# Kernel tuning notes

Hardware: AMD Instinct MI355X
Metric: run time of the kernel (lower is better)

The kernel has to match this reference:

```python
import jax, jax.numpy as jnp
import numpy as np

B, N_C, N_T, D, DF = 16, 2048, 1024, 2, 2
K, E_OBS = 16, 4
H, DH = 4, 16
F = H * DH  # 64-dim node features (embed_all output)


def setup_inputs() -> dict:
    key = jax.random.key(0)
    ks = jax.random.split(key, 16)
    r = lambda i, shape: jax.random.normal(ks[i], shape, jnp.float32) * 0.05
    d_in = E_OBS + D + DF  # obs(4) + s(2) + f(2) = 8
    return dict(
        s_ctx=jax.random.normal(ks[0], (B, N_C, D), jnp.float32),
        f_ctx=jax.random.normal(ks[1], (B, N_C, DF), jnp.float32),
        s_test=jax.random.normal(ks[2], (B, N_T, D), jnp.float32),
        emb_obs=r(3, (2, E_OBS)),
        W1=r(4, (d_in, 256)), b1=jnp.zeros((256,), jnp.float32),
        W2=r(5, (256, 128)), b2=jnp.zeros((128,), jnp.float32),
        W3=r(6, (128, F)), b3=jnp.zeros((F,), jnp.float32),
        ln_g=jnp.ones((F,), jnp.float32), ln_b=jnp.zeros((F,), jnp.float32),
        Wg=r(7, (F, F)),
        a_src=r(8, (H, DH)), a_dst=r(9, (H, DH)),
        We=r(10, (D, H)), be=jnp.zeros((H,), jnp.float32),
        H1=r(11, (F, 256)), c1=jnp.zeros((256,), jnp.float32),
        H2=r(12, (256, 64)), c2=jnp.zeros((64,), jnp.float32),
        H3=r(13, (64, 2)), c3=jnp.zeros((2,), jnp.float32),
    )


def _knn(q, ctx, k):
    # q [B,Nq,D], ctx [B,Nc,D] -> neighbor indices [B,Nq,K] and displacement edge feats [B,Nq,K,D]
    d2 = (jnp.sum(q * q, -1)[:, :, None] + jnp.sum(ctx * ctx, -1)[:, None, :]
          - 2.0 * jnp.einsum('bqd,bcd->bqc', q, ctx))
    _, idx = jax.lax.top_k(-d2, k)
    nb = jax.vmap(lambda c, i: c[i])(ctx, idx)  # gather neighbor coords per batch
    return idx, q[:, :, None, :] - nb


def _mlp3(x, W1, b1, W2, b2, W3, b3):
    x = jax.nn.gelu(x @ W1 + b1)
    x = jax.nn.gelu(x @ W2 + b2)
    return x @ W3 + b3


def _ln(x, g, b):
    mu = jnp.mean(x, -1, keepdims=True)
    v = jnp.var(x, -1, keepdims=True)
    return (x - mu) * jax.lax.rsqrt(v + 1e-6) * g + b


def reference(s_ctx, f_ctx, s_test, emb_obs, W1, b1, W2, b2, W3, b3, ln_g, ln_b,
              Wg, a_src, a_dst, We, be, H1, c1, H2, c2, H3, c3):
    # --- build kNN graph (ctx->ctx and ctx->test edges, K per receiver) ---
    s_cc, d_cc = _knn(s_ctx, s_ctx, K)
    s_ct, d_ct = _knn(s_test, s_ctx, K)
    edges = jnp.concatenate([d_cc.reshape(-1, D), d_ct.reshape(-1, D)], axis=0)  # [E, D]
    off = (jnp.arange(B) * N_C)[:, None, None]
    senders = jnp.concatenate([(s_cc + off).reshape(-1), (s_ct + off).reshape(-1)])  # [E]
    # receivers == repeat(arange(N), K): edges are grouped K-per-node in node order.

    # --- node embedding: [obs_embed | s | f] -> MLP -> LayerNorm ---
    ctx_in = jnp.concatenate([jnp.broadcast_to(emb_obs[1], (B, N_C, E_OBS)), s_ctx, f_ctx], -1)
    test_in = jnp.concatenate([jnp.broadcast_to(emb_obs[0], (B, N_T, E_OBS)), s_test,
                               jnp.zeros((B, N_T, DF), s_test.dtype)], -1)
    n_ctx = _ln(_mlp3(ctx_in, W1, b1, W2, b2, W3, b3), ln_g, ln_b)
    n_test = _ln(_mlp3(test_in, W1, b1, W2, b2, W3, b3), ln_g, ln_b)
    nodes = jnp.concatenate([n_ctx.reshape(B * N_C, F), n_test.reshape(B * N_T, F)], 0)
    N = B * (N_C + N_T)

    # --- edge-biased GAT message passing (K incoming edges per node) ---
    xp = (nodes @ Wg).reshape(N, H, DH)
    msg = xp[senders].reshape(N, K, H, DH)  # gather sender features
    sc = (jnp.einsum('nkhd,hd->nkh', msg, a_src)
          + jnp.einsum('nhd,hd->nh', xp, a_dst)[:, None, :])
    sc = jax.nn.leaky_relu(sc, 0.2) + (edges @ We + be).reshape(N, K, H)  # edge bias
    alpha = jax.nn.softmax(sc, axis=1)  # softmax over the K neighbors
    out = jnp.einsum('nkh,nkhd->nhd', alpha, msg).reshape(N, F)
    nodes = nodes + out  # residual

    # --- head on test nodes + diagonal MVN output ---
    n_t = nodes[-B * N_T:].reshape(B, N_T, F)
    o = jax.nn.gelu(n_t @ H1 + c1)
    o = jax.nn.gelu(o @ H2 + c2)
    o = o @ H3 + c3  # [B, N_t, 2]
    mean = o[..., 0:1]
    scale = jax.nn.softplus(o[..., 1:2])
    return jnp.concatenate([mean, scale], -1)
```

## Files before the change

### kernel.cpp

```cpp
#include <hip/hip_runtime.h>
#include <math.h>

#define NB 16
#define NCTX 2048
#define NTEST 1024
#define NCTX_TOT (NB*NCTX)
#define NTEST_TOT (NB*NTEST)
#define NTOT (NCTX_TOT + NTEST_TOT)

typedef _Float16 half8 __attribute__((ext_vector_type(8)));
typedef _Float16 half4 __attribute__((ext_vector_type(4)));
typedef float f32x4 __attribute__((ext_vector_type(4)));

__device__ __forceinline__ float gelu_f(float x) {
  float x3 = x * x * x;
  float y = 0.7978845608028654f * fmaf(0.044715f, x3, x);
  float e = __expf(2.0f * y);
  float th = 1.0f - 2.0f * __builtin_amdgcn_rcpf(e + 1.0f);
  return 0.5f * x * (1.0f + th);
}

__device__ __forceinline__ void fma4(float4& a, float s, float4 w) {
  a.x = fmaf(s, w.x, a.x);
  a.y = fmaf(s, w.y, a.y);
  a.z = fmaf(s, w.z, a.z);
  a.w = fmaf(s, w.w, a.w);
}

__device__ __forceinline__ float4 ldg4(const float* p) {
  return *reinterpret_cast<const float4*>(p);
}

__device__ __forceinline__ unsigned fkey(float f) {
  unsigned u = __float_as_uint(f);
  return (u & 0x80000000u) ? ~u : (u ^ 0x80000000u);
}
__device__ __forceinline__ float unfkey(unsigned k) {
  return (k & 0x80000000u) ? __uint_as_float(k ^ 0x80000000u)
                           : __uint_as_float(~k);
}

__global__ __launch_bounds__(256) void prep_kernel(
    const float* __restrict__ W1, const float* __restrict__ b1,
    const float* __restrict__ emb,
    const float* __restrict__ W2, const float* __restrict__ W3,
    const float* __restrict__ Wg,
    const float* __restrict__ H1, const float* __restrict__ H2,
    _Float16* __restrict__ W2P, _Float16* __restrict__ W3P,
    _Float16* __restrict__ WgP,
    _Float16* __restrict__ H1P, _Float16* __restrict__ H2P,
    float* __restrict__ ctype)
{
  int t = blockIdx.x * 256 + threadIdx.x;
  {
    int j = t >> 9, ks = (t >> 6) & 7, l = t & 63;
    int col = 16*j + (l & 15);
    int k0  = ks*32 + (l >> 4)*8;
    half8 o;
    #pragma unroll
    for (int e = 0; e < 8; ++e) o[e] = (_Float16)W2[(k0 + e)*128 + col];
    *reinterpret_cast<half8*>(&W2P[(size_t)t*8]) = o;
  }
  if (t < 1024) {
    int j = t >> 8, ks = (t >> 6) & 3, l = t & 63;
    int col = 16*j + (l & 15);
    int k0  = ks*32 + (l >> 4)*8;
    half8 o;
    #pragma unroll
    for (int e = 0; e < 8; ++e) o[e] = (_Float16)W3[(k0 + e)*64 + col];
    *reinterpret_cast<half8*>(&W3P[(size_t)t*8]) = o;
  }
  if (t < 512) {
    int j = t >> 7, ks = (t >> 6) & 1, l = t & 63;
    int col = 16*j + (l & 15);
    int k0  = ks*32 + (l >> 4)*8;
    half8 o;
    #pragma unroll
    for (int e = 0; e < 8; ++e) o[e] = (_Float16)Wg[(k0 + e)*64 + col];
    *reinterpret_cast<half8*>(&WgP[(size_t)t*8]) = o;
  }
  if (t < 2048) {
    int j = t >> 7, ks = (t >> 6) & 1, l = t & 63;
    int col = 16*j + (l & 15);
    int k0  = ks*32 + (l >> 4)*8;
    half8 o;
    #pragma unroll
    for (int e = 0; e < 8; ++e) o[e] = (_Float16)H1[(k0 + e)*256 + col];
    *reinterpret_cast<half8*>(&H1P[(size_t)t*8]) = o;
  }
  if (t < 2048) {
    int j = t >> 9, ks = (t >> 6) & 7, l = t & 63;
    int col = 16*j + (l & 15);
    int k0  = ks*32 + (l >> 4)*8;
    half8 o;
    #pragma unroll
    for (int e = 0; e < 8; ++e) o[e] = (_Float16)H2[(k0 + e)*64 + col];
    *reinterpret_cast<half8*>(&H2P[(size_t)t*8]) = o;
  }
  if (t < 512) {
    int ty = t >> 8, c = t & 255;
    float acc = b1[c];
    #pragma unroll
    for (int k = 0; k < 4; ++k) acc = fmaf(emb[ty*4 + k], W1[k*256 + c], acc);
    ctype[t] = acc;
  }
}

__global__ __launch_bounds__(256, 6) void knn_kernel(
    const float* __restrict__ s_ctx, const float* __restrict__ s_test,
    int* __restrict__ senders)
{
  __shared__ __align__(16) unsigned long long sk[4][128];
  const int t    = threadIdx.x;
  const int lane = t & 63;
  const int w    = t >> 6;
  const int blk  = blockIdx.x;
  const int bb   = blk >> 8;
  const int q    = (blk & 255) * 4 + w;
  const int trow = bb * NTEST + q;

  const float* cb = s_ctx + (size_t)bb * NCTX * 2;
  const float qx = s_test[(size_t)trow*2];
  const float qy = s_test[(size_t)trow*2 + 1];
  const float qq = __fadd_rn(__fmul_rn(qx,qx), __fmul_rn(qy,qy));

  float d[32];
  float mn = 3.4e38f;
  #pragma unroll
  for (int it = 0; it < 32; ++it) {
    float2 p = *reinterpret_cast<const float2*>(&cb[2*(it*64 + lane)]);
    float ss  = __fadd_rn(__fmul_rn(p.x,p.x), __fmul_rn(p.y,p.y));
    float dot = __fadd_rn(__fmul_rn(qx, p.x), __fmul_rn(qy, p.y));
    float d2  = __fsub_rn(__fadd_rn(qq, ss), __fmul_rn(2.0f, dot));
    d[it] = d2;
    mn = fminf(mn, d2);
  }

  unsigned key = fkey(mn);
  unsigned acc = 0u;
  #pragma unroll
  for (int bit = 31; bit >= 0; --bit) {
    unsigned candv = acc | (1u << bit);
    unsigned long long bal = __ballot(key < candv);
    if (__popcll(bal) < 16) acc = candv;
  }
  const float Tf = unfkey(acc);

  int base = 0;
  #pragma unroll
  for (int it = 0; it < 32; ++it) {
    bool pr = (d[it] <= Tf);
    unsigned long long m = __ballot(pr);
    if (pr) {
      int pos = base + __popcll(m & ((1ULL << lane) - 1ULL));
      if (pos < 128)
        sk[w][pos] = ((unsigned long long)fkey(d[it]) << 32)
                   | (unsigned)(it*64 + lane);
    }
    base += __popcll(m);
  }
  const int S = base;

  if (S <= 32) {
    if (lane >= S && lane < 32) sk[w][lane] = ~0ULL;
    unsigned long long pm = sk[w][lane & 31];
    int r0 = 0;
    #pragma unroll
    for (int j = 0; j < 32; ++j)
      r0 += (int)(sk[w][j] < pm);
    if (lane < S && r0 < 16)
      senders[(size_t)trow*16 + r0] = bb*NCTX + (int)(pm & 0xFFFFFFFFu);
  } else if (S <= 128) {
    unsigned long long p0 = (lane      < S) ? sk[w][lane]      : ~0ULL;
    unsigned long long p1 = (lane + 64 < S) ? sk[w][lane + 64] : ~0ULL;
    int r0 = 0, r1 = 0;
    for (int j = 0; j < S; ++j) {
      unsigned long long kj = sk[w][j];
      r0 += (int)(kj < p0);
      r1 += (int)(kj < p1);
    }
    if (lane < S && r0 < 16)
      senders[(size_t)trow*16 + r0] = bb*NCTX + (int)(p0 & 0xFFFFFFFFu);
    if (lane + 64 < S && r1 < 16)
      senders[(size_t)trow*16 + r1] = bb*NCTX + (int)(p1 & 0xFFFFFFFFu);
  } else {
    if (lane == 0) {
      float dist[16]; int ind[16];
      #pragma unroll
      for (int j=0;j<16;++j){ dist[j]=3.4e38f; ind[j]=0; }
      for (int c = 0; c < NCTX; ++c) {
        float2 p = *reinterpret_cast<const float2*>(&cb[2*c]);
        float ss  = __fadd_rn(__fmul_rn(p.x,p.x), __fmul_rn(p.y,p.y));
        float dot = __fadd_rn(__fmul_rn(qx, p.x), __fmul_rn(qy, p.y));
        float d2  = __fsub_rn(__fadd_rn(qq, ss), __fmul_rn(2.0f, dot));
        if (d2 < dist[15]) {
          float dj = d2; int ij = c;
          #pragma unroll
          for (int j = 0; j < 16; ++j) {
            bool sw = dj < dist[j];
            float td = dist[j]; int ti = ind[j];
            dist[j] = sw ? dj : td;  ind[j] = sw ? ij : ti;
            dj = sw ? td : dj;       ij = sw ? ti : ij;
          }
        }
      }
      for (int j = 0; j < 16; ++j)
        senders[(size_t)trow*16 + j] = bb*NCTX + ind[j];
    }
  }
}

__global__ __launch_bounds__(256, 4) void mlp_kernel(
    const float* __restrict__ s_ctx, const float* __restrict__ f_ctx,
    const float* __restrict__ s_test,
    const float* __restrict__ ctype, const float* __restrict__ W1,
    const _Float16* __restrict__ W2P, const float* __restrict__ b2,
    const _Float16* __restrict__ W3P, const float* __restrict__ b3,
    const float* __restrict__ ln_g, const float* __restrict__ ln_b,
    const _Float16* __restrict__ WgP,
    const float* __restrict__ a_src, const float* __restrict__ a_dst,
    float* __restrict__ nodes, _Float16* __restrict__ xph,
    float* __restrict__ xps, float* __restrict__ xpd)
{
  __shared__ __align__(16) char smem[34816];
  const int t    = threadIdx.x;
  const int lane = t & 63;
  const int w    = t >> 6;
  const int id   = blockIdx.x;
  char* slice = smem + w * 8704;
  _Float16* h1t  = reinterpret_cast<_Float16*>(slice);
  float (*xin)[4] = reinterpret_cast<float(*)[4]>(slice + 8448);
  _Float16* h2   = h1t;
  _Float16* nodh = h1t + 16*136;
  const int cn = lane & 15;
  const int kg = lane >> 4;
  const int m0 = (id*4 + w) * 16;
  const bool is_ctx = (m0 < NCTX_TOT);

  const _Float16* bQ2 = W2P + lane*8;
  const _Float16* bQ3 = W3P + lane*8;
  const _Float16* bQg = WgP + lane*8;

  half8 bb2[8];
  #pragma unroll
  for (int j = 0; j < 8; ++j)
    bb2[j] = *reinterpret_cast<const half8*>(bQ2 + j*4096);

  {
    int r = lane >> 2, c = lane & 3;
    int n = m0 + r;
    float v;
    if (is_ctx) v = (c < 2) ? s_ctx[2*(size_t)n + c] : f_ctx[2*(size_t)n + (c-2)];
    else { int tn = n - NCTX_TOT; v = (c < 2) ? s_test[2*(size_t)tn + c] : 0.f; }
    xin[r][c] = v;
  }

  {
    const int c0 = lane * 4;
    float4 w4 = ldg4(&W1[4*256 + c0]);
    float4 w5 = ldg4(&W1[5*256 + c0]);
    float4 w6 = ldg4(&W1[6*256 + c0]);
    float4 w7 = ldg4(&W1[7*256 + c0]);
    float4 cbv = ldg4(&ctype[(is_ctx ? 256 : 0) + c0]);
    #pragma unroll
    for (int r = 0; r < 16; ++r) {
      float4 xi = *reinterpret_cast<const float4*>(&xin[r][0]);
      float4 a = cbv;
      fma4(a, xi.x, w4); fma4(a, xi.y, w5);
      fma4(a, xi.z, w6); fma4(a, xi.w, w7);
      half4 o = { (_Float16)gelu_f(a.x), (_Float16)gelu_f(a.y),
                  (_Float16)gelu_f(a.z), (_Float16)gelu_f(a.w) };
      *reinterpret_cast<half4*>(&h1t[r*264 + c0]) = o;
    }
  }

  {
    f32x4 acc[8];
    #pragma unroll
    for (int j = 0; j < 8; ++j) {
      float bv = b2[16*j + cn];
      acc[j] = (f32x4){bv, bv, bv, bv};
    }
    const _Float16* aP = h1t + cn*264 + kg*8;
    #pragma unroll
    for (int ks = 0; ks < 8; ++ks) {
      half8 a = *reinterpret_cast<const half8*>(aP + ks*32);
      half8 bn[8];
      if (ks < 7) {
        #pragma unroll
        for (int j = 0; j < 8; ++j)
          bn[j] = *reinterpret_cast<const half8*>(bQ2 + j*4096 + (ks+1)*512);
      }
      #pragma unroll
      for (int j = 0; j < 8; ++j)
        acc[j] = __builtin_amdgcn_mfma_f32_16x16x32_f16(a, bb2[j], acc[j], 0, 0, 0);
      if (ks < 7) {
        #pragma unroll
        for (int j = 0; j < 8; ++j) bb2[j] = bn[j];
      }
    }
    #pragma unroll
    for (int j = 0; j < 8; ++j)
      #pragma unroll
      for (int r = 0; r < 4; ++r) {
        int m = kg*4 + r;
        h2[m*136 + 16*j + cn] = (_Float16)gelu_f(acc[j][r]);
      }
  }

  {
    f32x4 acc[4];
    #pragma unroll
    for (int j = 0; j < 4; ++j) {
      float bv = b3[16*j + cn];
      acc[j] = (f32x4){bv, bv, bv, bv};
    }
    const _Float16* aP = h2 + cn*136 + kg*8;
    half8 bb[4];
    #pragma unroll
    for (int j = 0; j < 4; ++j)
      bb[j] = *reinterpret_cast<const half8*>(bQ3 + j*2048);
    #pragma unroll
    for (int ks = 0; ks < 4; ++ks) {
      half8 a = *reinterpret_cast<const half8*>(aP + ks*32);
      half8 bn[4];
      if (ks < 3) {
        #pragma unroll
        for (int j = 0; j < 4; ++j)
          bn[j] = *reinterpret_cast<const half8*>(bQ3 + j*2048 + (ks+1)*512);
      }
      #pragma unroll
      for (int j = 0; j < 4; ++j)
        acc[j] = __builtin_amdgcn_mfma_f32_16x16x32_f16(a, bb[j], acc[j], 0, 0, 0);
      if (ks < 3) {
        #pragma unroll
        for (int j = 0; j < 4; ++j) bb[j] = bn[j];
      }
    }
    float gv[4], bvv[4];
    #pragma unroll
    for (int j = 0; j < 4; ++j) { gv[j] = ln_g[16*j+cn]; bvv[j] = ln_b[16*j+cn]; }
    const bool is_test = !is_ctx;
    #pragma unroll
    for (int r = 0; r < 4; ++r) {
      float sv = 0.f, sq = 0.f;
      #pragma unroll
      for (int j = 0; j < 4; ++j) {
        float v = acc[j][r];
        sv += v; sq += v*v;
      }
      #pragma unroll
      for (int o = 1; o < 16; o <<= 1) {
        sv += __shfl_xor(sv, o);
        sq += __shfl_xor(sq, o);
      }
      float mean = sv * (1.0f/64.0f);
      float var  = sq * (1.0f/64.0f) - mean*mean;
      float rstd = rsqrtf(var + 1e-6f);
      int m = kg*4 + r;
      #pragma unroll
      for (int j = 0; j < 4; ++j) {
        float v = (acc[j][r] - mean) * rstd * gv[j] + bvv[j];
        nodh[m*72 + 16*j + cn] = (_Float16)v;
        if (is_test)
          nodes[(size_t)(m0 + m)*64 + 16*j + cn] = v;
      }
    }
  }

  {
    f32x4 acc[4];
    #pragma unroll
    for (int j = 0; j < 4; ++j) acc[j] = (f32x4){0.f, 0.f, 0.f, 0.f};
    const _Float16* aP = nodh + cn*72 + kg*8;
    half8 bg0[4], bg1[4];
    #pragma unroll
    for (int j = 0; j < 4; ++j) {
      bg0[j] = *reinterpret_cast<const half8*>(bQg + j*1024);
      bg1[j] = *reinterpret_cast<const half8*>(bQg + j*1024 + 512);
    }
    half8 a0 = *reinterpret_cast<const half8*>(aP);
    half8 a1 = *reinterpret_cast<const half8*>(aP + 32);
    #pragma unroll
    for (int j = 0; j < 4; ++j)
      acc[j] = __builtin_amdgcn_mfma_f32_16x16x32_f16(a0, bg0[j], acc[j], 0, 0, 0);
    #pragma unroll
    for (int j = 0; j < 4; ++j)
      acc[j] = __builtin_amdgcn_mfma_f32_16x16x32_f16(a1, bg1[j], acc[j], 0, 0, 0);
    #pragma unroll
    for (int r = 0; r < 4; ++r) {
      int m = kg*4 + r;
      #pragma unroll
      for (int j = 0; j < 4; ++j)
        xph[(size_t)(m0 + m)*64 + 16*j + cn] = (_Float16)acc[j][r];
    }
    const float* av = is_ctx ? a_src : a_dst;
    float av0 = av[cn], av1 = av[16+cn], av2 = av[32+cn], av3 = av[48+cn];
    #pragma unroll
    for (int r = 0; r < 4; ++r) {
      float p0 = acc[0][r]*av0, p1 = acc[1][r]*av1;
      float p2 = acc[2][r]*av2, p3 = acc[3][r]*av3;
      #pragma unroll
      for (int o = 1; o < 16; o <<= 1) {
        p0 += __shfl_xor(p0, o); p1 += __shfl_xor(p1, o);
        p2 += __shfl_xor(p2, o); p3 += __shfl_xor(p3, o);
      }
      if (cn == 0) {
        int m = kg*4 + r;
        float4 v = make_float4(p0, p1, p2, p3);
        if (is_ctx)
          *reinterpret_cast<float4*>(&xps[(size_t)(m0 + m)*4]) = v;
        else
          *reinterpret_cast<float4*>(&xpd[(size_t)(m0 + m - NCTX_TOT)*4]) = v;
      }
    }
  }
}

__global__ __launch_bounds__(64, 3) void back_kernel(
    const float* __restrict__ s_ctx, const float* __restrict__ s_test,
    const _Float16* __restrict__ xph, const int* __restrict__ senders,
    const float* __restrict__ xps, const float* __restrict__ xpd,
    const float* __restrict__ We, const float* __restrict__ be,
    const float* __restrict__ nodes,
    const _Float16* __restrict__ H1P, const float* __restrict__ c1,
    const _Float16* __restrict__ H2P, const float* __restrict__ c2,
    const float* __restrict__ H3, const float* __restrict__ c3,
    float* __restrict__ outp)
{
  __shared__ __align__(16) _Float16 xinh[16*72];
  __shared__ __align__(16) _Float16 h1[16*264];
  const int lane = threadIdx.x;
  const int cn   = lane & 15;
  const int kg   = lane >> 4;
  const int bid  = blockIdx.x;
  const int L    = (bid & 7)*256 + (bid >> 3);
  const int row0 = L * 8;

  #pragma unroll
  for (int rr = 8; rr < 16; ++rr) xinh[rr*72 + lane] = (_Float16)0.f;

  {
    const int h  = kg;
    const int kk = cn;
    const int hb = lane & 48;
    const float we0 = We[h], we1 = We[4+h], beh = be[h];
    for (int rr = 0; rr < 8; ++rr) {
      const int trow = row0 + rr;
      int s = senders[(size_t)trow*16 + kk];
      s = (s < 0) ? 0 : ((s >= NCTX_TOT) ? NCTX_TOT - 1 : s);
      float pre = xps[(size_t)s*4 + h] + xpd[(size_t)trow*4 + h];
      float lr  = pre >= 0.f ? pre : 0.2f * pre;
      const float qx = s_test[(size_t)trow*2];
      const float qy = s_test[(size_t)trow*2 + 1];
      float ex = qx - s_ctx[(size_t)s*2];
      float ey = qy - s_ctx[(size_t)s*2 + 1];
      float sc = lr + fmaf(ex, we0, fmaf(ey, we1, beh));
      float mx = sc;
      #pragma unroll
      for (int o = 1; o < 16; o <<= 1) mx = fmaxf(mx, __shfl_xor(mx, o));
      float e = __expf(sc - mx);
      float sum = e;
      #pragma unroll
      for (int o = 1; o < 16; o <<= 1) sum += __shfl_xor(sum, o);
      float alpha = e / sum;
      float outv = 0.f;
      #pragma unroll
      for (int k = 0; k < 16; ++k) {
        int   sk = __shfl(s, k);
        float al = __shfl(alpha, hb + k);
        outv = fmaf(al, (float)xph[(size_t)sk*64 + lane], outv);
      }
      float xv = nodes[(size_t)(NCTX_TOT + trow)*64 + lane] + outv;
      xinh[rr*72 + lane] = (_Float16)xv;
    }
  }

  {
    const _Float16* aP  = xinh + cn*72 + kg*8;
    const _Float16* bQ1 = H1P + lane*8;
    half8 a0 = *reinterpret_cast<const half8*>(aP);
    half8 a1 = *reinterpret_cast<const half8*>(aP + 32);
    #pragma unroll
    for (int g = 0; g < 2; ++g) {
      f32x4 acc[8];
      #pragma unroll
      for (int j = 0; j < 8; ++j) {
        float bv = c1[16*(g*8 + j) + cn];
        acc[j] = (f32x4){bv, bv, bv, bv};
      }
      half8 b0[8], b1[8];
      #pragma unroll
      for (int j = 0; j < 8; ++j) {
        b0[j] = *reinterpret_cast<const half8*>(bQ1 + ((g*8 + j)*2 + 0)*512);
        b1[j] = *reinterpret_cast<const half8*>(bQ1 + ((g*8 + j)*2 + 1)*512);
      }
      #pragma unroll
      for (int j = 0; j < 8; ++j)
        acc[j] = __builtin_amdgcn_mfma_f32_16x16x32_f16(a0, b0[j], acc[j], 0, 0, 0);
      #pragma unroll
      for (int j = 0; j < 8; ++j)
        acc[j] = __builtin_amdgcn_mfma_f32_16x16x32_f16(a1, b1[j], acc[j], 0, 0, 0);
      #pragma unroll
      for (int j = 0; j < 8; ++j)
        #pragma unroll
        for (int r = 0; r < 4; ++r)
          h1[(kg*4 + r)*264 + 16*(g*8 + j) + cn] = (_Float16)gelu_f(acc[j][r]);
    }
  }

  {
    f32x4 acc[4];
    #pragma unroll
    for (int j = 0; j < 4; ++j) {
      float bv = c2[16*j + cn];
      acc[j] = (f32x4){bv, bv, bv, bv};
    }
    const _Float16* aP  = h1 + cn*264 + kg*8;
    const _Float16* bQ2 = H2P + lane*8;
    half8 bb[4];
    #pragma unroll
    for (int j = 0; j < 4; ++j)
      bb[j] = *reinterpret_cast<const half8*>(bQ2 + j*4096);
    #pragma unroll
    for (int ks = 0; ks < 8; ++ks) {
      half8 a = *reinterpret_cast<const half8*>(aP + ks*32);
      half8 bn[4];
      if (ks < 7) {
        #pragma unroll
        for (int j = 0; j < 4; ++j)
          bn[j] = *reinterpret_cast<const half8*>(bQ2 + j*4096 + (ks+1)*512);
      }
      #pragma unroll
      for (int j = 0; j < 4; ++j)
        acc[j] = __builtin_amdgcn_mfma_f32_16x16x32_f16(a, bb[j], acc[j], 0, 0, 0);
      if (ks < 7) {
        #pragma unroll
        for (int j = 0; j < 4; ++j) bb[j] = bn[j];
      }
    }
    float h30[4], h31[4];
    #pragma unroll
    for (int j = 0; j < 4; ++j) {
      h30[j] = H3[(16*j + cn)*2 + 0];
      h31[j] = H3[(16*j + cn)*2 + 1];
    }
    const float c30 = c3[0], c31 = c3[1];
    #pragma unroll
    for (int r = 0; r < 4; ++r) {
      float p0 = 0.f, p1 = 0.f;
      #pragma unroll
      for (int j = 0; j < 4; ++j) {
        float g = gelu_f(acc[j][r]);
        p0 = fmaf(g, h30[j], p0);
        p1 = fmaf(g, h31[j], p1);
      }
      #pragma unroll
      for (int o = 1; o < 16; o <<= 1) {
        p0 += __shfl_xor(p0, o);
        p1 += __shfl_xor(p1, o);
      }
      if (cn == 0 && kg < 2) {
        int row = row0 + kg*4 + r;
        float m = p0 + c30;
        float sa = p1 + c31;
        float sv = fmaxf(sa, 0.f) + log1pf(__expf(-fabsf(sa)));
        outp[(size_t)row*2 + 0] = m;
        outp[(size_t)row*2 + 1] = sv;
      }
    }
  }
}

extern "C" void kernel_launch(void* const* d_in, const int* in_sizes, int n_in,
                              void* d_out, int out_size, void* d_ws, size_t ws_size,
                              hipStream_t stream) {
  const float* s_ctx  = (const float*)d_in[0];
  const float* f_ctx  = (const float*)d_in[1];
  const float* s_test = (const float*)d_in[2];
  const float* emb    = (const float*)d_in[3];
  const float* W1 = (const float*)d_in[4];
  const float* b1 = (const float*)d_in[5];
  const float* W2 = (const float*)d_in[6];
  const float* b2 = (const float*)d_in[7];
  const float* W3 = (const float*)d_in[8];
  const float* b3 = (const float*)d_in[9];
  const float* ln_g = (const float*)d_in[10];
  const float* ln_b = (const float*)d_in[11];
  const float* Wg = (const float*)d_in[12];
  const float* a_src = (const float*)d_in[13];
  const float* a_dst = (const float*)d_in[14];
  const float* We = (const float*)d_in[15];
  const float* be = (const float*)d_in[16];
  const float* H1 = (const float*)d_in[17];
  const float* c1 = (const float*)d_in[18];
  const float* H2 = (const float*)d_in[19];
  const float* c2 = (const float*)d_in[20];
  const float* H3 = (const float*)d_in[21];
  const float* c3 = (const float*)d_in[22];

  float* nodes   = (float*)d_ws;
  _Float16* xph  = (_Float16*)(nodes + (size_t)NTOT*64);
  int*   senders = (int*)(xph + (size_t)NTOT*64);
  _Float16* W2P  = (_Float16*)(senders + (size_t)NTEST_TOT*16);
  _Float16* W3P  = W2P + 32768;
  _Float16* WgP  = W3P + 8192;
  _Float16* H1P  = WgP + 4096;
  _Float16* H2P  = H1P + 16384;
  float*   ctype = (float*)(H2P + 16384);
  float*   xps   = ctype + 512;
  float*   xpd   = xps + (size_t)NCTX_TOT*4;
  float* outp    = (float*)d_out;

  hipLaunchKernelGGL(prep_kernel, dim3(16), dim3(256), 0, stream,
                     W1, b1, emb, W2, W3, Wg, H1, H2,
                     W2P, W3P, WgP, H1P, H2P, ctype);
  hipLaunchKernelGGL(knn_kernel, dim3(4096), dim3(256), 0, stream,
                     s_ctx, s_test, senders);
  hipLaunchKernelGGL(mlp_kernel, dim3(768), dim3(256), 0, stream,
                     s_ctx, f_ctx, s_test, ctype, W1,
                     W2P, b2, W3P, b3, ln_g, ln_b, WgP,
                     a_src, a_dst, nodes, xph, xps, xpd);
  hipLaunchKernelGGL(back_kernel, dim3(2048), dim3(64), 0, stream,
                     s_ctx, s_test, xph, senders, xps, xpd, We, be,
                     nodes, H1P, c1, H2P, c2, H3, c3, outp);
}
```

Before: 76.96 us.

## Fuse prep, kNN and node MLP kernels into one block-partitioned front kernel

Merges the weight-prep, kNN and node-embedding MLP kernels into one launch, with each block choosing its role from its block index. The MLP blocks now convert W2/W3/Wg fp32 weights to fp16 MFMA fragments directly from global memory and recompute the type-bias instead of reading prepacked buffers. The intent is to remove two kernel launches and the serial dependency between prep, kNN and MLP so the independent stages overlap. In exchange, each MLP block does strided fp32 weight loads and conversions, and the fused kernel carries the larger register footprint of both code paths. It also adds an mbcnt-based prefix count and skips empty ballots in the kNN compaction.

```diff
diff --git a/kernel.cpp b/kernel.cpp
--- a/kernel.cpp
+++ b/kernel.cpp
@@ -40,379 +40,358 @@
                            : __uint_as_float(~k);
 }
 
-__global__ __launch_bounds__(256) void prep_kernel(
+__device__ __forceinline__ half8 packfrag(const float* __restrict__ W,
+                                          const int N, const int row0,
+                                          const int col) {
+  const float* p = W + (size_t)row0 * N + col;
+  half8 o;
+  #pragma unroll
+  for (int e = 0; e < 8; ++e) o[e] = (_Float16)p[e*N];
+  return o;
+}
+
+__global__ __launch_bounds__(256, 4) void front_kernel(
+    const float* __restrict__ s_ctx, const float* __restrict__ f_ctx,
+    const float* __restrict__ s_test, int* __restrict__ senders,
     const float* __restrict__ W1, const float* __restrict__ b1,
     const float* __restrict__ emb,
-    const float* __restrict__ W2, const float* __restrict__ W3,
+    const float* __restrict__ W2, const float* __restrict__ b2,
+    const float* __restrict__ W3, const float* __restrict__ b3,
+    const float* __restrict__ ln_g, const float* __restrict__ ln_b,
     const float* __restrict__ Wg,
+    const float* __restrict__ a_src, const float* __restrict__ a_dst,
     const float* __restrict__ H1, const float* __restrict__ H2,
-    _Float16* __restrict__ W2P, _Float16* __restrict__ W3P,
-    _Float16* __restrict__ WgP,
     _Float16* __restrict__ H1P, _Float16* __restrict__ H2P,
-    float* __restrict__ ctype)
-{
-  int t = blockIdx.x * 256 + threadIdx.x;
-  {
-    int j = t >> 9, ks = (t >> 6) & 7, l = t & 63;
-    int col = 16*j + (l & 15);
-    int k0  = ks*32 + (l >> 4)*8;
-    half8 o;
-    #pragma unroll
-    for (int e = 0; e < 8; ++e) o[e] = (_Float16)W2[(k0 + e)*128 + col];
-    *reinterpret_cast<half8*>(&W2P[(size_t)t*8]) = o;
-  }
-  if (t < 1024) {
-    int j = t >> 8, ks = (t >> 6) & 3, l = t & 63;
-    int col = 16*j + (l & 15);
-    int k0  = ks*32 + (l >> 4)*8;
-    half8 o;
-    #pragma unroll
-    for (int e = 0; e < 8; ++e) o[e] = (_Float16)W3[(k0 + e)*64 + col];
-    *reinterpret_cast<half8*>(&W3P[(size_t)t*8]) = o;
-  }
-  if (t < 512) {
-    int j = t >> 7, ks = (t >> 6) & 1, l = t & 63;
-    int col = 16*j + (l & 15);
-    int k0  = ks*32 + (l >> 4)*8;
-    half8 o;
-    #pragma unroll
-    for (int e = 0; e < 8; ++e) o[e] = (_Float16)Wg[(k0 + e)*64 + col];
-    *reinterpret_cast<half8*>(&WgP[(size_t)t*8]) = o;
-  }
-  if (t < 2048) {
-    int j = t >> 7, ks = (t >> 6) & 1, l = t & 63;
-    int col = 16*j + (l & 15);
-    int k0  = ks*32 + (l >> 4)*8;
-    half8 o;
-    #pragma unroll
-    for (int e = 0; e < 8; ++e) o[e] = (_Float16)H1[(k0 + e)*256 + col];
-    *reinterpret_cast<half8*>(&H1P[(size_t)t*8]) = o;
-  }
-  if (t < 2048) {
-    int j = t >> 9, ks = (t >> 6) & 7, l = t & 63;
-    int col = 16*j + (l & 15);
-    int k0  = ks*32 + (l >> 4)*8;
-    half8 o;
-    #pragma unroll
-    for (int e = 0; e < 8; ++e) o[e] = (_Float16)H2[(k0 + e)*64 + col];
-    *reinterpret_cast<half8*>(&H2P[(size_t)t*8]) = o;
-  }
-  if (t < 512) {
-    int ty = t >> 8, c = t & 255;
-    float acc = b1[c];
-    #pragma unroll
-    for (int k = 0; k < 4; ++k) acc = fmaf(emb[ty*4 + k], W1[k*256 + c], acc);
-    ctype[t] = acc;
-  }
-}
-
-__global__ __launch_bounds__(256, 6) void knn_kernel(
-    const float* __restrict__ s_ctx, const float* __restrict__ s_test,
-    int* __restrict__ senders)
-{
-  __shared__ __align__(16) unsigned long long sk[4][128];
-  const int t    = threadIdx.x;
-  const int lane = t & 63;
-  const int w    = t >> 6;
-  const int blk  = blockIdx.x;
-  const int bb   = blk >> 8;
-  const int q    = (blk & 255) * 4 + w;
-  const int trow = bb * NTEST + q;
-
-  const float* cb = s_ctx + (size_t)bb * NCTX * 2;
-  const float qx = s_test[(size_t)trow*2];
-  const float qy = s_test[(size_t)trow*2 + 1];
-  const float qq = __fadd_rn(__fmul_rn(qx,qx), __fmul_rn(qy,qy));
-
-  float d[32];
-  float mn = 3.4e38f;
-  #pragma unroll
-  for (int it = 0; it < 32; ++it) {
-    float2 p = *reinterpret_cast<const float2*>(&cb[2*(it*64 + lane)]);
-    float ss  = __fadd_rn(__fmul_rn(p.x,p.x), __fmul_rn(p.y,p.y));
-    float dot = __fadd_rn(__fmul_rn(qx, p.x), __fmul_rn(qy, p.y));
-    float d2  = __fsub_rn(__fadd_rn(qq, ss), __fmul_rn(2.0f, dot));
-    d[it] = d2;
-    mn = fminf(mn, d2);
-  }
-
-  unsigned key = fkey(mn);
-  unsigned acc = 0u;
-  #pragma unroll
-  for (int bit = 31; bit >= 0; --bit) {
-    unsigned candv = acc | (1u << bit);
-    unsigned long long bal = __ballot(key < candv);
-    if (__popcll(bal) < 16) acc = candv;
-  }
-  const float Tf = unfkey(acc);
-
-  int base = 0;
-  #pragma unroll
-  for (int it = 0; it < 32; ++it) {
-    bool pr = (d[it] <= Tf);
-    unsigned long long m = __ballot(pr);
-    if (pr) {
-      int pos = base + __popcll(m & ((1ULL << lane) - 1ULL));
-      if (pos < 128)
-        sk[w][pos] = ((unsigned long long)fkey(d[it]) << 32)
-                   | (unsigned)(it*64 + lane);
-    }
-    base += __popcll(m);
-  }
-  const int S = base;
-
-  if (S <= 32) {
-    if (lane >= S && lane < 32) sk[w][lane] = ~0ULL;
-    unsigned long long pm = sk[w][lane & 31];
-    int r0 = 0;
-    #pragma unroll
-    for (int j = 0; j < 32; ++j)
-      r0 += (int)(sk[w][j] < pm);
-    if (lane < S && r0 < 16)
-      senders[(size_t)trow*16 + r0] = bb*NCTX + (int)(pm & 0xFFFFFFFFu);
-  } else if (S <= 128) {
-    unsigned long long p0 = (lane      < S) ? sk[w][lane]      : ~0ULL;
-    unsigned long long p1 = (lane + 64 < S) ? sk[w][lane + 64] : ~0ULL;
-    int r0 = 0, r1 = 0;
-    for (int j = 0; j < S; ++j) {
-      unsigned long long kj = sk[w][j];
-      r0 += (int)(kj < p0);
-      r1 += (int)(kj < p1);
-    }
-    if (lane < S && r0 < 16)
-      senders[(size_t)trow*16 + r0] = bb*NCTX + (int)(p0 & 0xFFFFFFFFu);
-    if (lane + 64 < S && r1 < 16)
-      senders[(size_t)trow*16 + r1] = bb*NCTX + (int)(p1 & 0xFFFFFFFFu);
-  } else {
-    if (lane == 0) {
-      float dist[16]; int ind[16];
-      #pragma unroll
-      for (int j=0;j<16;++j){ dist[j]=3.4e38f; ind[j]=0; }
-      for (int c = 0; c < NCTX; ++c) {
-        float2 p = *reinterpret_cast<const float2*>(&cb[2*c]);
-        float ss  = __fadd_rn(__fmul_rn(p.x,p.x), __fmul_rn(p.y,p.y));
-        float dot = __fadd_rn(__fmul_rn(qx, p.x), __fmul_rn(qy, p.y));
-        float d2  = __fsub_rn(__fadd_rn(qq, ss), __fmul_rn(2.0f, dot));
-        if (d2 < dist[15]) {
-          float dj = d2; int ij = c;
-          #pragma unroll
-          for (int j = 0; j < 16; ++j) {
-            bool sw = dj < dist[j];
-            float td = dist[j]; int ti = ind[j];
-            dist[j] = sw ? dj : td;  ind[j] = sw ? ij : ti;
-            dj = sw ? td : dj;       ij = sw ? ti : ij;
-          }
-        }
-      }
-      for (int j = 0; j < 16; ++j)
-        senders[(size_t)trow*16 + j] = bb*NCTX + ind[j];
-    }
-  }
-}
-
-__global__ __launch_bounds__(256, 4) void mlp_kernel(
-    const float* __restrict__ s_ctx, const float* __restrict__ f_ctx,
-    const float* __restrict__ s_test,
-    const float* __restrict__ ctype, const float* __restrict__ W1,
-    const _Float16* __restrict__ W2P, const float* __restrict__ b2,
-    const _Float16* __restrict__ W3P, const float* __restrict__ b3,
-    const float* __restrict__ ln_g, const float* __restrict__ ln_b,
-    const _Float16* __restrict__ WgP,
-    const float* __restrict__ a_src, const float* __restrict__ a_dst,
     float* __restrict__ nodes, _Float16* __restrict__ xph,
     float* __restrict__ xps, float* __restrict__ xpd)
 {
   __shared__ __align__(16) char smem[34816];
+  const int blk  = blockIdx.x;
   const int t    = threadIdx.x;
   const int lane = t & 63;
   const int w    = t >> 6;
-  const int id   = blockIdx.x;
-  char* slice = smem + w * 8704;
-  _Float16* h1t  = reinterpret_cast<_Float16*>(slice);
-  float (*xin)[4] = reinterpret_cast<float(*)[4]>(slice + 8448);
-  _Float16* h2   = h1t;
-  _Float16* nodh = h1t + 16*136;
-  const int cn = lane & 15;
-  const int kg = lane >> 4;
-  const int m0 = (id*4 + w) * 16;
-  const bool is_ctx = (m0 < NCTX_TOT);
-
-  const _Float16* bQ2 = W2P + lane*8;
-  const _Float16* bQ3 = W3P + lane*8;
-  const _Float16* bQg = WgP + lane*8;
-
-  half8 bb2[8];
-  #pragma unroll
-  for (int j = 0; j < 8; ++j)
-    bb2[j] = *reinterpret_cast<const half8*>(bQ2 + j*4096);
-
-  {
-    int r = lane >> 2, c = lane & 3;
-    int n = m0 + r;
-    float v;
-    if (is_ctx) v = (c < 2) ? s_ctx[2*(size_t)n + c] : f_ctx[2*(size_t)n + (c-2)];
-    else { int tn = n - NCTX_TOT; v = (c < 2) ? s_test[2*(size_t)tn + c] : 0.f; }
-    xin[r][c] = v;
-  }
-
-  {
-    const int c0 = lane * 4;
-    float4 w4 = ldg4(&W1[4*256 + c0]);
-    float4 w5 = ldg4(&W1[5*256 + c0]);
-    float4 w6 = ldg4(&W1[6*256 + c0]);
-    float4 w7 = ldg4(&W1[7*256 + c0]);
-    float4 cbv = ldg4(&ctype[(is_ctx ? 256 : 0) + c0]);
-    #pragma unroll
-    for (int r = 0; r < 16; ++r) {
-      float4 xi = *reinterpret_cast<const float4*>(&xin[r][0]);
-      float4 a = cbv;
-      fma4(a, xi.x, w4); fma4(a, xi.y, w5);
-      fma4(a, xi.z, w6); fma4(a, xi.w, w7);
-      half4 o = { (_Float16)gelu_f(a.x), (_Float16)gelu_f(a.y),
-                  (_Float16)gelu_f(a.z), (_Float16)gelu_f(a.w) };
-      *reinterpret_cast<half4*>(&h1t[r*264 + c0]) = o;
-    }
-  }
-
-  {
-    f32x4 acc[8];
-    #pragma unroll
-    for (int j = 0; j < 8; ++j) {
-      float bv = b2[16*j + cn];
-      acc[j] = (f32x4){bv, bv, bv, bv};
-    }
-    const _Float16* aP = h1t + cn*264 + kg*8;
-    #pragma unroll
-    for (int ks = 0; ks < 8; ++ks) {
-      half8 a = *reinterpret_cast<const half8*>(aP + ks*32);
-      half8 bn[8];
-      if (ks < 7) {
+
+  if (blk < 4096) {
+    unsigned long long (*sk)[128] =
+        reinterpret_cast<unsigned long long(*)[128]>(smem);
+    const int bb   = blk >> 8;
+    const int q    = (blk & 255) * 4 + w;
+    const int trow = bb * NTEST + q;
+
+    const float* cb = s_ctx + (size_t)bb * NCTX * 2;
+    const float qx = s_test[(size_t)trow*2];
+    const float qy = s_test[(size_t)trow*2 + 1];
+    const float qq = __fadd_rn(__fmul_rn(qx,qx), __fmul_rn(qy,qy));
+
+    float d[32];
+    float mn = 3.4e38f;
+    #pragma unroll
+    for (int it = 0; it < 32; ++it) {
+      float2 p = *reinterpret_cast<const float2*>(&cb[2*(it*64 + lane)]);
+      float ss  = __fadd_rn(__fmul_rn(p.x,p.x), __fmul_rn(p.y,p.y));
+      float dot = __fadd_rn(__fmul_rn(qx, p.x), __fmul_rn(qy, p.y));
+      float d2  = __fsub_rn(__fadd_rn(qq, ss), __fmul_rn(2.0f, dot));
+      d[it] = d2;
+      mn = fminf(mn, d2);
+    }
+
+    unsigned key = fkey(mn);
+    unsigned acc = 0u;
+    #pragma unroll
+    for (int bit = 31; bit >= 0; --bit) {
+      unsigned candv = acc | (1u << bit);
+      unsigned long long bal = __ballot(key < candv);
+      if (__popcll(bal) < 16) acc = candv;
+    }
+    const float Tf = unfkey(acc);
+
+    int base = 0;
+    #pragma unroll
+    for (int it = 0; it < 32; ++it) {
+      bool pr = (d[it] <= Tf);
+      unsigned long long m = __ballot(pr);
+      if (m != 0ULL) {
+        int mb = __builtin_amdgcn_mbcnt_hi(
+                   (unsigned)(m >> 32),
+                   __builtin_amdgcn_mbcnt_lo((unsigned)m, 0u));
+        if (pr) {
+          int pos = base + mb;
+          if (pos < 128)
+            sk[w][pos] = ((unsigned long long)fkey(d[it]) << 32)
+                       | (unsigned)(it*64 + lane);
+        }
+        base += __popcll(m);
+      }
+    }
+    const int S = base;
+
+    if (S <= 32) {
+      if (lane >= S && lane < 32) sk[w][lane] = ~0ULL;
+      unsigned long long pm = sk[w][lane & 31];
+      int r0 = 0;
+      #pragma unroll
+      for (int j = 0; j < 32; ++j)
+        r0 += (int)(sk[w][j] < pm);
+      if (lane < S && r0 < 16)
+        senders[(size_t)trow*16 + r0] = bb*NCTX + (int)(pm & 0xFFFFFFFFu);
+    } else if (S <= 128) {
+      unsigned long long p0 = (lane      < S) ? sk[w][lane]      : ~0ULL;
+      unsigned long long p1 = (lane + 64 < S) ? sk[w][lane + 64] : ~0ULL;
+      int r0 = 0, r1 = 0;
+      for (int j = 0; j < S; ++j) {
+        unsigned long long kj = sk[w][j];
+        r0 += (int)(kj < p0);
+        r1 += (int)(kj < p1);
+      }
+      if (lane < S && r0 < 16)
+        senders[(size_t)trow*16 + r0] = bb*NCTX + (int)(p0 & 0xFFFFFFFFu);
+      if (lane + 64 < S && r1 < 16)
+        senders[(size_t)trow*16 + r1] = bb*NCTX + (int)(p1 & 0xFFFFFFFFu);
+    } else {
+      if (lane == 0) {
+        float dist[16]; int ind[16];
+        #pragma unroll
+        for (int j=0;j<16;++j){ dist[j]=3.4e38f; ind[j]=0; }
+        for (int c = 0; c < NCTX; ++c) {
+          float2 p = *reinterpret_cast<const float2*>(&cb[2*c]);
+          float ss  = __fadd_rn(__fmul_rn(p.x,p.x), __fmul_rn(p.y,p.y));
+          float dot = __fadd_rn(__fmul_rn(qx, p.x), __fmul_rn(qy, p.y));
+          float d2  = __fsub_rn(__fadd_rn(qq, ss), __fmul_rn(2.0f, dot));
+          if (d2 < dist[15]) {
+            float dj = d2; int ij = c;
+            #pragma unroll
+            for (int j = 0; j < 16; ++j) {
+              bool sw = dj < dist[j];
+              float td = dist[j]; int ti = ind[j];
+              dist[j] = sw ? dj : td;  ind[j] = sw ? ij : ti;
+              dj = sw ? td : dj;       ij = sw ? ti : ij;
+            }
+          }
+        }
+        for (int j = 0; j < 16; ++j)
+          senders[(size_t)trow*16 + j] = bb*NCTX + ind[j];
+      }
+    }
+  } else if (blk < 4864) {
+    const int id = blk - 4096;
+    char* slice = smem + w * 8704;
+    _Float16* h1t  = reinterpret_cast<_Float16*>(slice);
+    float (*xin)[4] = reinterpret_cast<float(*)[4]>(slice + 8448);
+    _Float16* h2   = h1t;
+    _Float16* nodh = h1t + 16*136;
+    const int cn = lane & 15;
+    const int kg = lane >> 4;
+    const int m0 = (id*4 + w) * 16;
+    const bool is_ctx = (m0 < NCTX_TOT);
+    const int colb = lane & 15;
+    const int rowb = (lane >> 4) * 8;
+
+    half8 bb2[8];
+    #pragma unroll
+    for (int j = 0; j < 8; ++j)
+      bb2[j] = packfrag(W2, 128, rowb, 16*j + colb);
+
+    {
+      int r = lane >> 2, c = lane & 3;
+      int n = m0 + r;
+      float v;
+      if (is_ctx) v = (c < 2) ? s_ctx[2*(size_t)n + c] : f_ctx[2*(size_t)n + (c-2)];
+      else { int tn = n - NCTX_TOT; v = (c < 2) ? s_test[2*(size_t)tn + c] : 0.f; }
+      xin[r][c] = v;
+    }
+
+    {
+      const int c0 = lane * 4;
+      float4 w4 = ldg4(&W1[4*256 + c0]);
+      float4 w5 = ldg4(&W1[5*256 + c0]);
+      float4 w6 = ldg4(&W1[6*256 + c0]);
+      float4 w7 = ldg4(&W1[7*256 + c0]);
+      float4 cbv;
+      {
+        const int ty = is_ctx ? 1 : 0;
+        float* cv = reinterpret_cast<float*>(&cbv);
+        #pragma unroll
+        for (int u = 0; u < 4; ++u) {
+          int c = c0 + u;
+          float a = b1[c];
+          #pragma unroll
+          for (int k = 0; k < 4; ++k)
+            a = fmaf(emb[ty*4 + k], W1[k*256 + c], a);
+          cv[u] = a;
+        }
+      }
+      #pragma unroll
+      for (int r = 0; r < 16; ++r) {
+        float4 xi = *reinterpret_cast<const float4*>(&xin[r][0]);
+        float4 a = cbv;
+        fma4(a, xi.x, w4); fma4(a, xi.y, w5);
+        fma4(a, xi.z, w6); fma4(a, xi.w, w7);
+        half4 o = { (_Float16)gelu_f(a.x), (_Float16)gelu_f(a.y),
+                    (_Float16)gelu_f(a.z), (_Float16)gelu_f(a.w) };
+        *reinterpret_cast<half4*>(&h1t[r*264 + c0]) = o;
+      }
+    }
+
+    {
+      f32x4 acc[8];
+      #pragma unroll
+      for (int j = 0; j < 8; ++j) {
+        float bv = b2[16*j + cn];
+        acc[j] = (f32x4){bv, bv, bv, bv};
+      }
+      const _Float16* aP = h1t + cn*264 + kg*8;
+      #pragma unroll
+      for (int ks = 0; ks < 8; ++ks) {
+        half8 a = *reinterpret_cast<const half8*>(aP + ks*32);
+        half8 bn[8];
+        if (ks < 7) {
+          #pragma unroll
+          for (int j = 0; j < 8; ++j)
+            bn[j] = packfrag(W2, 128, (ks+1)*32 + rowb, 16*j + colb);
+        }
         #pragma unroll
         for (int j = 0; j < 8; ++j)
-          bn[j] = *reinterpret_cast<const half8*>(bQ2 + j*4096 + (ks+1)*512);
+          acc[j] = __builtin_amdgcn_mfma_f32_16x16x32_f16(a, bb2[j], acc[j], 0, 0, 0);
+        if (ks < 7) {
+          #pragma unroll
+          for (int j = 0; j < 8; ++j) bb2[j] = bn[j];
+        }
       }
       #pragma unroll
       for (int j = 0; j < 8; ++j)
-        acc[j] = __builtin_amdgcn_mfma_f32_16x16x32_f16(a, bb2[j], acc[j], 0, 0, 0);
-      if (ks < 7) {
-        #pragma unroll
-        for (int j = 0; j < 8; ++j) bb2[j] = bn[j];
-      }
-    }
-    #pragma unroll
-    for (int j = 0; j < 8; ++j)
+        #pragma unroll
+        for (int r = 0; r < 4; ++r) {
+          int m = kg*4 + r;
+          h2[m*136 + 16*j + cn] = (_Float16)gelu_f(acc[j][r]);
+        }
+    }
+
+    {
+      f32x4 acc[4];
+      #pragma unroll
+      for (int j = 0; j < 4; ++j) {
+        float bv = b3[16*j + cn];
+        acc[j] = (f32x4){bv, bv, bv, bv};
+      }
+      const _Float16* aP = h2 + cn*136 + kg*8;
+      half8 bb[4];
+      #pragma unroll
+      for (int j = 0; j < 4; ++j)
+        bb[j] = packfrag(W3, 64, rowb, 16*j + colb);
+      #pragma unroll
+      for (int ks = 0; ks < 4; ++ks) {
+        half8 a = *reinterpret_cast<const half8*>(aP + ks*32);
+        half8 bn[4];
+        if (ks < 3) {
+          #pragma unroll
+          for (int j = 0; j < 4; ++j)
+            bn[j] = packfrag(W3, 64, (ks+1)*32 + rowb, 16*j + colb);
+        }
+        #pragma unroll
+        for (int j = 0; j < 4; ++j)
+          acc[j] = __builtin_amdgcn_mfma_f32_16x16x32_f16(a, bb[j], acc[j], 0, 0, 0);
+        if (ks < 3) {
+          #pragma unroll
+          for (int j = 0; j < 4; ++j) bb[j] = bn[j];
+        }
+      }
+      float gv[4], bvv[4];
+      #pragma unroll
+      for (int j = 0; j < 4; ++j) { gv[j] = ln_g[16*j+cn]; bvv[j] = ln_b[16*j+cn]; }
+      const bool is_test = !is_ctx;
+      #pragma unroll
+      for (int r = 0; r < 4; ++r) {
+        float sv = 0.f, sq = 0.f;
+        #pragma unroll
+        for (int j = 0; j < 4; ++j) {
+          float v = acc[j][r];
+          sv += v; sq += v*v;
+        }
+        #pragma unroll
+        for (int o = 1; o < 16; o <<= 1) {
+          sv += __shfl_xor(sv, o);
+          sq += __shfl_xor(sq, o);
+        }
+        float mean = sv * (1.0f/64.0f);
+        float var  = sq * (1.0f/64.0f) - mean*mean;
+        float rstd = rsqrtf(var + 1e-6f);
+        int m = kg*4 + r;
+        #pragma unroll
+        for (int j = 0; j < 4; ++j) {
+          float v = (acc[j][r] - mean) * rstd * gv[j] + bvv[j];
+          nodh[m*72 + 16*j + cn] = (_Float16)v;
+          if (is_test)
+            nodes[(size_t)(m0 + m)*64 + 16*j + cn] = v;
+        }
+      }
+    }
+
+    {
+      f32x4 acc[4];
+      #pragma unroll
+      for (int j = 0; j < 4; ++j) acc[j] = (f32x4){0.f, 0.f, 0.f, 0.f};
+      const _Float16* aP = nodh + cn*72 + kg*8;
+      half8 bg0[4], bg1[4];
+      #pragma unroll
+      for (int j = 0; j < 4; ++j) {
+        bg0[j] = packfrag(Wg, 64, rowb,      16*j + colb);
+        bg1[j] = packfrag(Wg, 64, 32 + rowb, 16*j + colb);
+      }
+      half8 a0 = *reinterpret_cast<const half8*>(aP);
+      half8 a1 = *reinterpret_cast<const half8*>(aP + 32);
+      #pragma unroll
+      for (int j = 0; j < 4; ++j)
+        acc[j] = __builtin_amdgcn_mfma_f32_16x16x32_f16(a0, bg0[j], acc[j], 0, 0, 0);
+      #pragma unroll
+      for (int j = 0; j < 4; ++j)
+        acc[j] = __builtin_amdgcn_mfma_f32_16x16x32_f16(a1, bg1[j], acc[j], 0, 0, 0);
       #pragma unroll
       for (int r = 0; r < 4; ++r) {
         int m = kg*4 + r;
-        h2[m*136 + 16*j + cn] = (_Float16)gelu_f(acc[j][r]);
-      }
-  }
-
-  {
-    f32x4 acc[4];
-    #pragma unroll
-    for (int j = 0; j < 4; ++j) {
-      float bv = b3[16*j + cn];
-      acc[j] = (f32x4){bv, bv, bv, bv};
-    }
-    const _Float16* aP = h2 + cn*136 + kg*8;
-    half8 bb[4];
-    #pragma unroll
-    for (int j = 0; j < 4; ++j)
-      bb[j] = *reinterpret_cast<const half8*>(bQ3 + j*2048);
-    #pragma unroll
-    for (int ks = 0; ks < 4; ++ks) {
-      half8 a = *reinterpret_cast<const half8*>(aP + ks*32);
-      half8 bn[4];
-      if (ks < 3) {
         #pragma unroll
         for (int j = 0; j < 4; ++j)
-          bn[j] = *reinterpret_cast<const half8*>(bQ3 + j*2048 + (ks+1)*512);
-      }
-      #pragma unroll
-      for (int j = 0; j < 4; ++j)
-        acc[j] = __builtin_amdgcn_mfma_f32_16x16x32_f16(a, bb[j], acc[j], 0, 0, 0);
-      if (ks < 3) {
-        #pragma unroll
-        for (int j = 0; j < 4; ++j) bb[j] = bn[j];
-      }
-    }
-    float gv[4], bvv[4];
-    #pragma unroll
-    for (int j = 0; j < 4; ++j) { gv[j] = ln_g[16*j+cn]; bvv[j] = ln_b[16*j+cn]; }
-    const bool is_test = !is_ctx;
-    #pragma unroll
-    for (int r = 0; r < 4; ++r) {
-      float sv = 0.f, sq = 0.f;
-      #pragma unroll
-      for (int j = 0; j < 4; ++j) {
-        float v = acc[j][r];
-        sv += v; sq += v*v;
-      }
-      #pragma unroll
-      for (int o = 1; o < 16; o <<= 1) {
-        sv += __shfl_xor(sv, o);
-        sq += __shfl_xor(sq, o);
-      }
-      float mean = sv * (1.0f/64.0f);
-      float var  = sq * (1.0f/64.0f) - mean*mean;
-      float rstd = rsqrtf(var + 1e-6f);
-      int m = kg*4 + r;
-      #pragma unroll
-      for (int j = 0; j < 4; ++j) {
-        float v = (acc[j][r] - mean) * rstd * gv[j] + bvv[j];
-        nodh[m*72 + 16*j + cn] = (_Float16)v;
-        if (is_test)
-          nodes[(size_t)(m0 + m)*64 + 16*j + cn] = v;
-      }
-    }
-  }
-
-  {
-    f32x4 acc[4];
-    #pragma unroll
-    for (int j = 0; j < 4; ++j) acc[j] = (f32x4){0.f, 0.f, 0.f, 0.f};
-    const _Float16* aP = nodh + cn*72 + kg*8;
-    half8 bg0[4], bg1[4];
-    #pragma unroll
-    for (int j = 0; j < 4; ++j) {
-      bg0[j] = *reinterpret_cast<const half8*>(bQg + j*1024);
-      bg1[j] = *reinterpret_cast<const half8*>(bQg + j*1024 + 512);
-    }
-    half8 a0 = *reinterpret_cast<const half8*>(aP);
-    half8 a1 = *reinterpret_cast<const half8*>(aP + 32);
-    #pragma unroll
-    for (int j = 0; j < 4; ++j)
-      acc[j] = __builtin_amdgcn_mfma_f32_16x16x32_f16(a0, bg0[j], acc[j], 0, 0, 0);
-    #pragma unroll
-    for (int j = 0; j < 4; ++j)
-      acc[j] = __builtin_amdgcn_mfma_f32_16x16x32_f16(a1, bg1[j], acc[j], 0, 0, 0);
-    #pragma unroll
-    for (int r = 0; r < 4; ++r) {
-      int m = kg*4 + r;
-      #pragma unroll
-      for (int j = 0; j < 4; ++j)
-        xph[(size_t)(m0 + m)*64 + 16*j + cn] = (_Float16)acc[j][r];
-    }
-    const float* av = is_ctx ? a_src : a_dst;
-    float av0 = av[cn], av1 = av[16+cn], av2 = av[32+cn], av3 = av[48+cn];
-    #pragma unroll
-    for (int r = 0; r < 4; ++r) {
-      float p0 = acc[0][r]*av0, p1 = acc[1][r]*av1;
-      float p2 = acc[2][r]*av2, p3 = acc[3][r]*av3;
-      #pragma unroll
-      for (int o = 1; o < 16; o <<= 1) {
-        p0 += __shfl_xor(p0, o); p1 += __shfl_xor(p1, o);
-        p2 += __shfl_xor(p2, o); p3 += __shfl_xor(p3, o);
-      }
-      if (cn == 0) {
-        int m = kg*4 + r;
-        float4 v = make_float4(p0, p1, p2, p3);
-        if (is_ctx)
-          *reinterpret_cast<float4*>(&xps[(size_t)(m0 + m)*4]) = v;
-        else
-          *reinterpret_cast<float4*>(&xpd[(size_t)(m0 + m - NCTX_TOT)*4]) = v;
-      }
+          xph[(size_t)(m0 + m)*64 + 16*j + cn] = (_Float16)acc[j][r];
+      }
+      const float* av = is_ctx ? a_src : a_dst;
+      float av0 = av[cn], av1 = av[16+cn], av2 = av[32+cn], av3 = av[48+cn];
+      #pragma unroll
+      for (int r = 0; r < 4; ++r) {
+        float p0 = acc[0][r]*av0, p1 = acc[1][r]*av1;
+        float p2 = acc[2][r]*av2, p3 = acc[3][r]*av3;
+        #pragma unroll
+        for (int o = 1; o < 16; o <<= 1) {
+          p0 += __shfl_xor(p0, o); p1 += __shfl_xor(p1, o);
+          p2 += __shfl_xor(p2, o); p3 += __shfl_xor(p3, o);
+        }
+        if (cn == 0) {
+          int m = kg*4 + r;
+          float4 v = make_float4(p0, p1, p2, p3);
+          if (is_ctx)
+            *reinterpret_cast<float4*>(&xps[(size_t)(m0 + m)*4]) = v;
+          else
+            *reinterpret_cast<float4*>(&xpd[(size_t)(m0 + m - NCTX_TOT)*4]) = v;
+        }
+      }
+    }
+  } else {
+    const int i = (blk - 4864)*256 + t;
+    if (i < 2048) {
+      int j = i >> 7, ks = (i >> 6) & 1, l = i & 63;
+      int col = 16*j + (l & 15);
+      int k0  = ks*32 + (l >> 4)*8;
+      half8 o;
+      #pragma unroll
+      for (int e = 0; e < 8; ++e) o[e] = (_Float16)H1[(k0 + e)*256 + col];
+      *reinterpret_cast<half8*>(&H1P[(size_t)i*8]) = o;
+    } else {
+      int i2 = i - 2048;
+      int j = i2 >> 9, ks = (i2 >> 6) & 7, l = i2 & 63;
+      int col = 16*j + (l & 15);
+      int k0  = ks*32 + (l >> 4)*8;
+      half8 o;
+      #pragma unroll
+      for (int e = 0; e < 8; ++e) o[e] = (_Float16)H2[(k0 + e)*64 + col];
+      *reinterpret_cast<half8*>(&H2P[(size_t)i2*8]) = o;
     }
   }
 }
@@ -607,20 +586,15 @@
   _Float16* WgP  = W3P + 8192;
   _Float16* H1P  = WgP + 4096;
   _Float16* H2P  = H1P + 16384;
-  float*   ctype = (float*)(H2P + 16384);
-  float*   xps   = ctype + 512;
+  float*   xps   = (float*)(H2P + 16384) + 512;
   float*   xpd   = xps + (size_t)NCTX_TOT*4;
   float* outp    = (float*)d_out;
 
-  hipLaunchKernelGGL(prep_kernel, dim3(16), dim3(256), 0, stream,
-                     W1, b1, emb, W2, W3, Wg, H1, H2,
-                     W2P, W3P, WgP, H1P, H2P, ctype);
-  hipLaunchKernelGGL(knn_kernel, dim3(4096), dim3(256), 0, stream,
-                     s_ctx, s_test, senders);
-  hipLaunchKernelGGL(mlp_kernel, dim3(768), dim3(256), 0, stream,
-                     s_ctx, f_ctx, s_test, ctype, W1,
-                     W2P, b2, W3P, b3, ln_g, ln_b, WgP,
-                     a_src, a_dst, nodes, xph, xps, xpd);
+  hipLaunchKernelGGL(front_kernel, dim3(4880), dim3(256), 0, stream,
+                     s_ctx, f_ctx, s_test, senders,
+                     W1, b1, emb, W2, b2, W3, b3, ln_g, ln_b, Wg,
+                     a_src, a_dst, H1, H2, H1P, H2P,
+                     nodes, xph, xps, xpd);
   hipLaunchKernelGGL(back_kernel, dim3(2048), dim3(64), 0, stream,
                      s_ctx, s_test, xph, senders, xps, xpd, We, be,
                      nodes, H1P, c1, H2P, c2, H3, c3, outp);
```

After: 88.58 us. 15.1% more time.
